# Kernel optimization log

Measured on AMD Instinct MI355X. Metric: run time of the kernel, lower is better.

## Reference

```python
import jax, jax.numpy as jnp
import numpy as np

B, S, V, E, H, T = 256, 160, 50000, 300, 256, 200

def setup_inputs() -> dict:
    key = jax.random.key(0)
    ks = jax.random.split(key, 12)
    return {
        'x1': jax.random.randint(ks[0], (B, S), 0, V),
        'x2': jax.random.randint(ks[1], (B, S), 0, V),
        'x1mask': jnp.ones((B, S), jnp.float32),
        'key_c': jax.random.normal(ks[2], (B, S, T), jnp.float32) * 0.1,
        'key_r': jax.random.normal(ks[3], (B, S, T), jnp.float32) * 0.1,
        'emb_table': jax.random.normal(ks[4], (V, E), jnp.float32) * 0.1,
        'W_ih': jax.random.normal(ks[5], (4 * H, E), jnp.float32) * 0.05,
        'W_hh': jax.random.normal(ks[6], (4 * H, H), jnp.float32) * 0.05,
        'W_kh': jax.random.normal(ks[7], (4 * H, T), jnp.float32) * 0.05,
        'b_g': jnp.zeros((4 * H,), jnp.float32),
        'W_attn': jax.random.normal(ks[8], (H, H), jnp.float32) * 0.05,
        'b_attn': jnp.zeros((H,), jnp.float32),
        'M': jax.random.normal(ks[9], (H, H), jnp.float32) * 0.05,
        'b': jnp.zeros((1,), jnp.float32),
    }

def _run_rnn(x_emb, k_emb, W_ih, W_hh, W_kh, b_g):
    # x_emb: [B,S,E], k_emb: [B,S,T] -> hidden states [B,S,H]
    Bn = x_emb.shape[0]
    h0 = jnp.zeros((Bn, H), x_emb.dtype)
    c0 = jnp.zeros((Bn, H), x_emb.dtype)
    def cell(carry, inp):
        h, c = carry
        x_t, k_t = inp
        g = x_t @ W_ih.T + h @ W_hh.T + k_t @ W_kh.T + b_g  # [B,4H]
        i, f, gg, o = jnp.split(g, 4, axis=-1)
        c = jax.nn.sigmoid(f) * c + jax.nn.sigmoid(i) * jnp.tanh(gg)
        h = jax.nn.sigmoid(o) * jnp.tanh(c)
        return (h, c), h
    xs = (jnp.swapaxes(x_emb, 0, 1), jnp.swapaxes(k_emb, 0, 1))  # time-major
    (_, _), hs = jax.lax.scan(cell, (h0, c0), xs)
    return jnp.swapaxes(hs, 0, 1)  # [B,S,H]

def reference(x1, x2, x1mask, key_c, key_r, emb_table, W_ih, W_hh, W_kh, b_g,
              W_attn, b_attn, M, b):
    x1_emb = emb_table[x1]  # [B,S,E] (dropout = identity at eval)
    x2_emb = emb_table[x2]
    sc = _run_rnn(x1_emb, key_c, W_ih, W_hh, W_kh, b_g)  # context states [B,S,H]
    rs = _run_rnn(x2_emb, key_r, W_ih, W_hh, W_kh, b_g)
    r = rs[:, -1]  # last response hidden [B,H]
    # masked dot-product attention over context states keyed by r
    attn = sc @ W_attn.T + b_attn  # [B,S,H]
    energies = jnp.einsum('bsh,bh->bs', attn, r) * x1mask
    alpha = jax.nn.softmax(energies, axis=-1)
    c_attn = jnp.einsum('bs,bsh->bh', alpha, sc)
    # bilinear score
    o = jnp.einsum('bh,hk,bk->b', c_attn, M, r) + b[0]
    return o
```

## Files before the change

### kernel.cpp

```cpp
#include <hip/hip_runtime.h>
#include <math.h>

#define B_   256
#define S_   160
#define E_   300
#define H_   256
#define T_   200
#define G4H  1024
#define CH   16
#define NCH  10

typedef float  f32x4  __attribute__((ext_vector_type(4)));
typedef __bf16 bf16x4 __attribute__((ext_vector_type(4)));
typedef __bf16 bf16x8 __attribute__((ext_vector_type(8)));

__device__ __forceinline__ float sigf(float x) {
    float e = expf(-fabsf(x));
    float p = 1.0f / (1.0f + e);
    return x >= 0.0f ? p : e * p;
}

__device__ __forceinline__ int norig(int np) {
    return ((np >> 4) & 3) * 256 + ((np >> 6) << 4) + (np & 15);
}

__device__ __forceinline__ float4 pick4(const float* __restrict__ e,
                                        const float* __restrict__ k, int kg) {
    if (kg < E_)      return *(const float4*)(e + kg);
    if (kg < E_ + T_) return *(const float4*)(k + (kg - E_));
    return make_float4(0.f, 0.f, 0.f, 0.f);
}

__device__ __forceinline__ void split4(float4 v, bf16x4& h, bf16x4& l) {
    h[0] = (__bf16)v.x; l[0] = (__bf16)(v.x - (float)h[0]);
    h[1] = (__bf16)v.y; l[1] = (__bf16)(v.y - (float)h[1]);
    h[2] = (__bf16)v.z; l[2] = (__bf16)(v.z - (float)h[2]);
    h[3] = (__bf16)v.w; l[3] = (__bf16)(v.w - (float)h[3]);
}

__global__ __launch_bounds__(128) void prep_split(
    const float* __restrict__ Whh, const float* __restrict__ Wih,
    const float* __restrict__ Wkh,
    __bf16* __restrict__ whh_hi, __bf16* __restrict__ whh_lo,
    __bf16* __restrict__ wik_hi, __bf16* __restrict__ wik_lo)
{
    const int n  = blockIdx.x;
    const int np = ((n & 255) >> 4) * 64 + (n >> 8) * 16 + (n & 15);
    const int t  = threadIdx.x;
    {
        const int k4 = t * 4;
        float4 v;
        if (k4 < E_)            v = *(const float4*)(Wih + (size_t)n * E_ + k4);
        else if (k4 < E_ + T_)  v = *(const float4*)(Wkh + (size_t)n * T_ + (k4 - E_));
        else                    v = make_float4(0.f, 0.f, 0.f, 0.f);
        bf16x4 h, l;
        split4(v, h, l);
        *(bf16x4*)(wik_hi + (size_t)np * 512 + k4) = h;
        *(bf16x4*)(wik_lo + (size_t)np * 512 + k4) = l;
    }
    if (t < 64) {
        const int k4 = t * 4;
        const float4 v = *(const float4*)(Whh + (size_t)n * 256 + k4);
        bf16x4 h, l;
        split4(v, h, l);
        *(bf16x4*)(whh_hi + (size_t)np * 256 + k4) = h;
        *(bf16x4*)(whh_lo + (size_t)np * 256 + k4) = l;
    }
}

__global__ __launch_bounds__(512, 2) void gemm_g2(
    const int* __restrict__ x1, const int* __restrict__ x2,
    const float* __restrict__ key_c, const float* __restrict__ key_r,
    const float* __restrict__ emb,
    const __bf16* __restrict__ wik_hi, const __bf16* __restrict__ wik_lo,
    const float* __restrict__ bg,
    float* __restrict__ G, int s0)
{
    __shared__ __align__(16) __bf16 Ah[128 * 32];
    __shared__ __align__(16) __bf16 Al[128 * 32];
    __shared__ __align__(16) __bf16 Bh[128 * 32];
    __shared__ __align__(16) __bf16 Bl[128 * 32];

    const int t   = threadIdx.x;
    const int rnn = blockIdx.z;
    const int m0  = blockIdx.x * 128;
    const int n0  = blockIdx.y * 128;
    const int* xx = rnn ? x2 : x1;
    const float* key = rnn ? key_r : key_c;

    const int r0 = t >> 2;
    const int cq = t & 3;
    const int csw = ((cq ^ ((r0 >> 1) & 3)) * 16);

    const float* aeb; const float* akb;
    const __bf16* wph; const __bf16* wpl;
    {
        const int am = m0 + r0;
        const int bs = (am >> 4) * S_ + s0 + (am & 15);
        aeb = emb + (size_t)xx[bs] * E_;
        akb = key + (size_t)bs * T_;
        wph = wik_hi + (size_t)(n0 + r0) * 512;
        wpl = wik_lo + (size_t)(n0 + r0) * 512;
    }

    const int w  = t >> 6;
    const int wm = w >> 2;
    const int wn = w & 3;
    const int l  = t & 63;
    const int cl = l & 15;
    const int ch = l >> 4;
    const int chs = ((ch ^ ((cl >> 1) & 3)) * 16);

    f32x4 acc[4][2];
    #pragma unroll
    for (int fm = 0; fm < 4; ++fm)
        #pragma unroll
        for (int fn = 0; fn < 2; ++fn) acc[fm][fn] = (f32x4){0.f, 0.f, 0.f, 0.f};

    for (int kt = 0; kt < 16; ++kt) {
        const int kg = kt * 32 + cq * 8;
        const float4 va0 = pick4(aeb, akb, kg);
        const float4 va1 = pick4(aeb, akb, kg + 4);
        const bf16x8 vbh = *(const bf16x8*)(wph + kg);
        const bf16x8 vbl = *(const bf16x8*)(wpl + kg);
        bf16x4 h0, l0, h1, l1;
        split4(va0, h0, l0);
        split4(va1, h1, l1);
        const bf16x8 sah = __builtin_shufflevector(h0, h1, 0, 1, 2, 3, 4, 5, 6, 7);
        const bf16x8 sal = __builtin_shufflevector(l0, l1, 0, 1, 2, 3, 4, 5, 6, 7);
        __syncthreads();
        {
            const int off = r0 * 64 + csw;
            *(bf16x8*)((char*)Ah + off) = sah;
            *(bf16x8*)((char*)Al + off) = sal;
            *(bf16x8*)((char*)Bh + off) = vbh;
            *(bf16x8*)((char*)Bl + off) = vbl;
        }
        __syncthreads();

        bf16x8 fBh[2], fBl[2];
        #pragma unroll
        for (int fn = 0; fn < 2; ++fn) {
            const int off = (wn * 32 + fn * 16 + cl) * 64 + chs;
            fBh[fn] = *(const bf16x8*)((const char*)Bh + off);
            fBl[fn] = *(const bf16x8*)((const char*)Bl + off);
        }
        #pragma unroll
        for (int fm = 0; fm < 4; ++fm) {
            const int off = (wm * 64 + fm * 16 + cl) * 64 + chs;
            const bf16x8 fAh = *(const bf16x8*)((const char*)Ah + off);
            const bf16x8 fAl = *(const bf16x8*)((const char*)Al + off);
            #pragma unroll
            for (int fn = 0; fn < 2; ++fn) {
                acc[fm][fn] = __builtin_amdgcn_mfma_f32_16x16x32_bf16(fAh, fBh[fn], acc[fm][fn], 0, 0, 0);
                acc[fm][fn] = __builtin_amdgcn_mfma_f32_16x16x32_bf16(fAh, fBl[fn], acc[fm][fn], 0, 0, 0);
                acc[fm][fn] = __builtin_amdgcn_mfma_f32_16x16x32_bf16(fAl, fBh[fn], acc[fm][fn], 0, 0, 0);
            }
        }
    }

    float bgl[2];
    #pragma unroll
    for (int fn = 0; fn < 2; ++fn)
        bgl[fn] = bg[norig(n0 + wn * 32 + fn * 16 + cl)];

    #pragma unroll
    for (int fm = 0; fm < 4; ++fm) {
        #pragma unroll
        for (int r = 0; r < 4; ++r) {
            const int m  = m0 + wm * 64 + fm * 16 + ch * 4 + r;
            const int b  = m >> 4;
            const int sl = m & 15;
            float* rowp = G + ((size_t)(rnn * CH + sl) * B_ + b) * G4H;
            #pragma unroll
            for (int fn = 0; fn < 2; ++fn)
                rowp[n0 + wn * 32 + fn * 16 + cl] = acc[fm][fn][r] + bgl[fn];
        }
    }
}

__global__ __launch_bounds__(512, 2) void lstm_ks(
    const float* __restrict__ G,
    const __bf16* __restrict__ Whi, const __bf16* __restrict__ Wlo,
    const __bf16* __restrict__ hhi_in, const __bf16* __restrict__ hlo_in,
    __bf16* __restrict__ hhi_out, __bf16* __restrict__ hlo_out,
    float* __restrict__ cst, float* __restrict__ sc,
    int sl, int s_glob, int first)
{
    __shared__ float ps[128 * 66];

    const int t  = threadIdx.x;
    const int w  = t >> 6;
    const int l  = t & 63;
    const int cl = l & 15;
    const int ch = l >> 4;
    const int mt = blockIdx.x;
    const int jt = blockIdx.y;
    const int rnn = mt >> 4;
    const int b0  = (mt & 15) * 16;
    const int m0  = mt * 16;

    const int me = (t >> 4) & 15;
    const int jl = t & 15;
    const int j  = jt * 16 + jl;
    float Ge[4];
    float c_in = 0.f;
    if (t < 256) {
        const float* Gb = G + ((size_t)(rnn * CH + sl) * B_ + b0 + me) * G4H + jt * 64;
        #pragma unroll
        for (int g = 0; g < 4; ++g) Ge[g] = Gb[g * 16 + jl];
        if (!first) c_in = cst[(size_t)(m0 + me) * 256 + j];
    }

    const size_t ab = (size_t)(m0 + cl) * 256 + w * 32 + ch * 8;
    const bf16x8 fAh = *(const bf16x8*)(hhi_in + ab);
    const bf16x8 fAl = *(const bf16x8*)(hlo_in + ab);

    bf16x8 fBh[4], fBl[4];
    #pragma unroll
    for (int g = 0; g < 4; ++g) {
        const size_t bb = (size_t)(jt * 64 + g * 16 + cl) * 256 + w * 32 + ch * 8;
        fBh[g] = *(const bf16x8*)(Whi + bb);
        fBl[g] = *(const bf16x8*)(Wlo + bb);
    }

    f32x4 acc[4];
    #pragma unroll
    for (int g = 0; g < 4; ++g) acc[g] = (f32x4){0.f, 0.f, 0.f, 0.f};
    #pragma unroll
    for (int g = 0; g < 4; ++g) {
        acc[g] = __builtin_amdgcn_mfma_f32_16x16x32_bf16(fAh, fBh[g], acc[g], 0, 0, 0);
        acc[g] = __builtin_amdgcn_mfma_f32_16x16x32_bf16(fAh, fBl[g], acc[g], 0, 0, 0);
        acc[g] = __builtin_amdgcn_mfma_f32_16x16x32_bf16(fAl, fBh[g], acc[g], 0, 0, 0);
    }

    #pragma unroll
    for (int g = 0; g < 4; ++g)
        #pragma unroll
        for (int r = 0; r < 4; ++r)
            ps[(w * 16 + ch * 4 + r) * 66 + g * 16 + cl] = acc[g][r];
    __syncthreads();

    if (t < 256) {
        float g4[4];
        #pragma unroll
        for (int g = 0; g < 4; ++g) {
            float s = Ge[g];
            #pragma unroll
            for (int w2 = 0; w2 < 8; ++w2)
                s += ps[(w2 * 16 + me) * 66 + g * 16 + jl];
            g4[g] = s;
        }
        const float c = sigf(g4[1]) * c_in + sigf(g4[0]) * tanhf(g4[2]);
        const float h = sigf(g4[3]) * tanhf(c);
        cst[(size_t)(m0 + me) * 256 + j] = c;
        const __bf16 hh = (__bf16)h;
        const size_t ho = (size_t)(m0 + me) * 256 + j;
        hhi_out[ho] = hh;
        hlo_out[ho] = (__bf16)(h - (float)hh);
        if (rnn == 0)
            sc[((size_t)(b0 + me) * S_ + s_glob) * H_ + j] = h;
    }
}

__global__ __launch_bounds__(256) void final_kernel(
    const float* __restrict__ sc,
    const __bf16* __restrict__ rhi, const __bf16* __restrict__ rlo,
    const float* __restrict__ Wattn, const float* __restrict__ battn,
    const float* __restrict__ M, const float* __restrict__ bscal,
    const float* __restrict__ mask, float* __restrict__ out)
{
    __shared__ float rs[256], us[256], red[256], as_[256];
    const int b = blockIdx.x;
    const int t = threadIdx.x;

    const size_t ri = (size_t)(256 + b) * 256 + t;
    rs[t] = (float)rhi[ri] + (float)rlo[ri];
    __syncthreads();

    float acc = 0.0f;
    for (int h = 0; h < 256; ++h) acc += rs[h] * Wattn[h * 256 + t];
    us[t] = acc;

    red[t] = battn[t] * rs[t];
    __syncthreads();
    for (int off = 128; off; off >>= 1) {
        if (t < off) red[t] += red[t + off];
        __syncthreads();
    }
    float beta = red[0];
    __syncthreads();

    float vh = 0.0f;
    {
        const float* Mrow = M + t * 256;
        for (int k = 0; k < 256; ++k) vh += Mrow[k] * rs[k];
    }

    float e = -INFINITY;
    if (t < S_) {
        float d = 0.0f;
        const float* scrow = sc + ((size_t)b * S_ + t) * H_;
        for (int h = 0; h < 256; ++h) d += scrow[h] * us[h];
        e = (d + beta) * mask[b * S_ + t];
    }
    red[t] = e;
    __syncthreads();
    for (int off = 128; off; off >>= 1) {
        if (t < off) red[t] = fmaxf(red[t], red[t + off]);
        __syncthreads();
    }
    float mx = red[0];
    __syncthreads();

    float p = (t < S_) ? expf(e - mx) : 0.0f;
    as_[t] = p;
    red[t] = p;
    __syncthreads();
    for (int off = 128; off; off >>= 1) {
        if (t < off) red[t] += red[t + off];
        __syncthreads();
    }
    float inv = 1.0f / red[0];
    __syncthreads();

    float ca = 0.0f;
    for (int s = 0; s < S_; ++s) ca += as_[s] * sc[((size_t)b * S_ + s) * H_ + t];
    ca *= inv;

    red[t] = ca * vh;
    __syncthreads();
    for (int off = 128; off; off >>= 1) {
        if (t < off) red[t] += red[t + off];
        __syncthreads();
    }
    if (t == 0) out[b] = red[0] + bscal[0];
}

extern "C" void kernel_launch(void* const* d_in, const int* in_sizes, int n_in,
                              void* d_out, int out_size, void* d_ws, size_t ws_size,
                              hipStream_t stream)
{
    const int*   x1    = (const int*)d_in[0];
    const int*   x2    = (const int*)d_in[1];
    const float* mask  = (const float*)d_in[2];
    const float* key_c = (const float*)d_in[3];
    const float* key_r = (const float*)d_in[4];
    const float* emb   = (const float*)d_in[5];
    const float* Wih   = (const float*)d_in[6];
    const float* Whh   = (const float*)d_in[7];
    const float* Wkh   = (const float*)d_in[8];
    const float* bg    = (const float*)d_in[9];
    const float* Wattn = (const float*)d_in[10];
    const float* battn = (const float*)d_in[11];
    const float* M     = (const float*)d_in[12];
    const float* bb    = (const float*)d_in[13];
    float* out = (float*)d_out;
    char*  wsb = (char*)d_ws;

    float*  G     = (float*)(wsb + 0);
    float*  sc    = (float*)(wsb + 33554432);
    __bf16* hhi0  = (__bf16*)(wsb + 75497472);
    __bf16* hlo0  = (__bf16*)(wsb + 75759616);
    __bf16* hhi1  = (__bf16*)(wsb + 76021760);
    __bf16* hlo1  = (__bf16*)(wsb + 76283904);
    float*  cst   = (float*)(wsb + 76546048);
    __bf16* WhhHi = (__bf16*)(wsb + 77070336);
    __bf16* WhhLo = (__bf16*)(wsb + 77594624);
    __bf16* WikHi = (__bf16*)(wsb + 78118912);
    __bf16* WikLo = (__bf16*)(wsb + 79167488);
    if (ws_size < 80216064) return;

    hipMemsetAsync(hhi0, 0, 524288, stream);
    prep_split<<<dim3(1024), 128, 0, stream>>>(Whh, Wih, Wkh,
                                               WhhHi, WhhLo, WikHi, WikLo);

    for (int ci = 0; ci < NCH; ++ci) {
        gemm_g2<<<dim3(32, 8, 2), 512, 0, stream>>>(x1, x2, key_c, key_r, emb,
                                                    WikHi, WikLo, bg, G, ci * CH);
        for (int slq = 0; slq < CH; ++slq) {
            const int s   = ci * CH + slq;
            const int par = s & 1;
            lstm_ks<<<dim3(32, 16), 512, 0, stream>>>(G, WhhHi, WhhLo,
                                                      par ? hhi1 : hhi0,
                                                      par ? hlo1 : hlo0,
                                                      par ? hhi0 : hhi1,
                                                      par ? hlo0 : hlo1,
                                                      cst, sc, slq, s, s == 0);
        }
    }

    final_kernel<<<dim3(256), 256, 0, stream>>>(sc, hhi0, hlo0, Wattn, battn,
                                                M, bb, mask, out);
}
```

Baseline: 1.508 ms.

## Use single-wave LSTM step blocks and widen GEMM K-tile to 64

The recurrent step kernel is rewritten so one 64-thread wave computes a full 16x64 gate tile over the whole K=256 reduction, instead of 8 waves each doing a K-slice and reducing partials through shared memory with a barrier. This drops the LDS reduction and block sync from the latency-bound per-timestep kernel, at the cost of a longer serial MFMA chain per wave and fewer threads per block. Separately, the input-projection GEMM now stages 64-wide K tiles with a new XOR swizzle, halving the number of barrier-separated iterations in exchange for more LDS.

New measurement: 1.901 ms. 26.1% more time.

```diff
diff --git a/kernel.cpp b/kernel.cpp
--- a/kernel.cpp
+++ b/kernel.cpp
@@ -76,10 +76,10 @@
     const float* __restrict__ bg,
     float* __restrict__ G, int s0)
 {
-    __shared__ __align__(16) __bf16 Ah[128 * 32];
-    __shared__ __align__(16) __bf16 Al[128 * 32];
-    __shared__ __align__(16) __bf16 Bh[128 * 32];
-    __shared__ __align__(16) __bf16 Bl[128 * 32];
+    __shared__ __align__(16) __bf16 Ah[128 * 64];
+    __shared__ __align__(16) __bf16 Al[128 * 64];
+    __shared__ __align__(16) __bf16 Bh[128 * 64];
+    __shared__ __align__(16) __bf16 Bl[128 * 64];
 
     const int t   = threadIdx.x;
     const int rnn = blockIdx.z;
@@ -90,7 +90,8 @@
 
     const int r0 = t >> 2;
     const int cq = t & 3;
-    const int csw = ((cq ^ ((r0 >> 1) & 3)) * 16);
+    const int p0 = (cq ^ (r0 & 7)) * 16;
+    const int p1 = ((cq + 4) ^ (r0 & 7)) * 16;
 
     const float* aeb; const float* akb;
     const __bf16* wph; const __bf16* wpl;
@@ -109,7 +110,6 @@
     const int l  = t & 63;
     const int cl = l & 15;
     const int ch = l >> 4;
-    const int chs = ((ch ^ ((cl >> 1) & 3)) * 16);
 
     f32x4 acc[4][2];
     #pragma unroll
@@ -117,44 +117,64 @@
         #pragma unroll
         for (int fn = 0; fn < 2; ++fn) acc[fm][fn] = (f32x4){0.f, 0.f, 0.f, 0.f};
 
-    for (int kt = 0; kt < 16; ++kt) {
-        const int kg = kt * 32 + cq * 8;
-        const float4 va0 = pick4(aeb, akb, kg);
-        const float4 va1 = pick4(aeb, akb, kg + 4);
-        const bf16x8 vbh = *(const bf16x8*)(wph + kg);
-        const bf16x8 vbl = *(const bf16x8*)(wpl + kg);
-        bf16x4 h0, l0, h1, l1;
-        split4(va0, h0, l0);
-        split4(va1, h1, l1);
-        const bf16x8 sah = __builtin_shufflevector(h0, h1, 0, 1, 2, 3, 4, 5, 6, 7);
-        const bf16x8 sal = __builtin_shufflevector(l0, l1, 0, 1, 2, 3, 4, 5, 6, 7);
+    for (int kt = 0; kt < 8; ++kt) {
+        const int kg0 = kt * 64 + cq * 8;
+        const int kg1 = kg0 + 32;
+        const float4 va0 = pick4(aeb, akb, kg0);
+        const float4 va1 = pick4(aeb, akb, kg0 + 4);
+        const float4 va2 = pick4(aeb, akb, kg1);
+        const float4 va3 = pick4(aeb, akb, kg1 + 4);
+        const bf16x8 vbh0 = *(const bf16x8*)(wph + kg0);
+        const bf16x8 vbh1 = *(const bf16x8*)(wph + kg1);
+        const bf16x8 vbl0 = *(const bf16x8*)(wpl + kg0);
+        const bf16x8 vbl1 = *(const bf16x8*)(wpl + kg1);
+        bf16x4 h0, l0, h1, l1, h2, l2, h3, l3;
+        split4(va0, h0, l0); split4(va1, h1, l1);
+        split4(va2, h2, l2); split4(va3, h3, l3);
+        const bf16x8 sah0 = __builtin_shufflevector(h0, h1, 0, 1, 2, 3, 4, 5, 6, 7);
+        const bf16x8 sal0 = __builtin_shufflevector(l0, l1, 0, 1, 2, 3, 4, 5, 6, 7);
+        const bf16x8 sah1 = __builtin_shufflevector(h2, h3, 0, 1, 2, 3, 4, 5, 6, 7);
+        const bf16x8 sal1 = __builtin_shufflevector(l2, l3, 0, 1, 2, 3, 4, 5, 6, 7);
         __syncthreads();
         {
-            const int off = r0 * 64 + csw;
-            *(bf16x8*)((char*)Ah + off) = sah;
-            *(bf16x8*)((char*)Al + off) = sal;
-            *(bf16x8*)((char*)Bh + off) = vbh;
-            *(bf16x8*)((char*)Bl + off) = vbl;
+            char* a = (char*)Ah + r0 * 128;
+            char* b = (char*)Bh + r0 * 128;
+            char* a2 = (char*)Al + r0 * 128;
+            char* b2 = (char*)Bl + r0 * 128;
+            *(bf16x8*)(a + p0)  = sah0;
+            *(bf16x8*)(a + p1)  = sah1;
+            *(bf16x8*)(a2 + p0) = sal0;
+            *(bf16x8*)(a2 + p1) = sal1;
+            *(bf16x8*)(b + p0)  = vbh0;
+            *(bf16x8*)(b + p1)  = vbh1;
+            *(bf16x8*)(b2 + p0) = vbl0;
+            *(bf16x8*)(b2 + p1) = vbl1;
         }
         __syncthreads();
 
-        bf16x8 fBh[2], fBl[2];
-        #pragma unroll
-        for (int fn = 0; fn < 2; ++fn) {
-            const int off = (wn * 32 + fn * 16 + cl) * 64 + chs;
-            fBh[fn] = *(const bf16x8*)((const char*)Bh + off);
-            fBl[fn] = *(const bf16x8*)((const char*)Bl + off);
-        }
-        #pragma unroll
-        for (int fm = 0; fm < 4; ++fm) {
-            const int off = (wm * 64 + fm * 16 + cl) * 64 + chs;
-            const bf16x8 fAh = *(const bf16x8*)((const char*)Ah + off);
-            const bf16x8 fAl = *(const bf16x8*)((const char*)Al + off);
+        #pragma unroll
+        for (int s = 0; s < 2; ++s) {
+            const int c = s * 4 + ch;
+            bf16x8 fBh[2], fBl[2];
             #pragma unroll
             for (int fn = 0; fn < 2; ++fn) {
-                acc[fm][fn] = __builtin_amdgcn_mfma_f32_16x16x32_bf16(fAh, fBh[fn], acc[fm][fn], 0, 0, 0);
-                acc[fm][fn] = __builtin_amdgcn_mfma_f32_16x16x32_bf16(fAh, fBl[fn], acc[fm][fn], 0, 0, 0);
-                acc[fm][fn] = __builtin_amdgcn_mfma_f32_16x16x32_bf16(fAl, fBh[fn], acc[fm][fn], 0, 0, 0);
+                const int row = wn * 32 + fn * 16 + cl;
+                const int off = row * 128 + (c ^ (row & 7)) * 16;
+                fBh[fn] = *(const bf16x8*)((const char*)Bh + off);
+                fBl[fn] = *(const bf16x8*)((const char*)Bl + off);
+            }
+            #pragma unroll
+            for (int fm = 0; fm < 4; ++fm) {
+                const int row = wm * 64 + fm * 16 + cl;
+                const int off = row * 128 + (c ^ (row & 7)) * 16;
+                const bf16x8 fAh = *(const bf16x8*)((const char*)Ah + off);
+                const bf16x8 fAl = *(const bf16x8*)((const char*)Al + off);
+                #pragma unroll
+                for (int fn = 0; fn < 2; ++fn) {
+                    acc[fm][fn] = __builtin_amdgcn_mfma_f32_16x16x32_bf16(fAh, fBh[fn], acc[fm][fn], 0, 0, 0);
+                    acc[fm][fn] = __builtin_amdgcn_mfma_f32_16x16x32_bf16(fAh, fBl[fn], acc[fm][fn], 0, 0, 0);
+                    acc[fm][fn] = __builtin_amdgcn_mfma_f32_16x16x32_bf16(fAl, fBh[fn], acc[fm][fn], 0, 0, 0);
+                }
             }
         }
     }
@@ -179,7 +199,7 @@
     }
 }
 
-__global__ __launch_bounds__(512, 2) void lstm_ks(
+__global__ __launch_bounds__(64) void lstm_dir(
     const float* __restrict__ G,
     const __bf16* __restrict__ Whi, const __bf16* __restrict__ Wlo,
     const __bf16* __restrict__ hhi_in, const __bf16* __restrict__ hlo_in,
@@ -187,79 +207,76 @@
     float* __restrict__ cst, float* __restrict__ sc,
     int sl, int s_glob, int first)
 {
-    __shared__ float ps[128 * 66];
-
-    const int t  = threadIdx.x;
-    const int w  = t >> 6;
-    const int l  = t & 63;
+    const int l  = threadIdx.x;
     const int cl = l & 15;
     const int ch = l >> 4;
-    const int mt = blockIdx.x;
-    const int jt = blockIdx.y;
+    const int bid = blockIdx.x;
+    const int mt  = bid >> 4;
+    const int jt  = bid & 15;
     const int rnn = mt >> 4;
     const int b0  = (mt & 15) * 16;
     const int m0  = mt * 16;
-
-    const int me = (t >> 4) & 15;
-    const int jl = t & 15;
-    const int j  = jt * 16 + jl;
-    float Ge[4];
-    float c_in = 0.f;
-    if (t < 256) {
-        const float* Gb = G + ((size_t)(rnn * CH + sl) * B_ + b0 + me) * G4H + jt * 64;
-        #pragma unroll
-        for (int g = 0; g < 4; ++g) Ge[g] = Gb[g * 16 + jl];
-        if (!first) c_in = cst[(size_t)(m0 + me) * 256 + j];
-    }
-
-    const size_t ab = (size_t)(m0 + cl) * 256 + w * 32 + ch * 8;
-    const bf16x8 fAh = *(const bf16x8*)(hhi_in + ab);
-    const bf16x8 fAl = *(const bf16x8*)(hlo_in + ab);
-
-    bf16x8 fBh[4], fBl[4];
-    #pragma unroll
-    for (int g = 0; g < 4; ++g) {
-        const size_t bb = (size_t)(jt * 64 + g * 16 + cl) * 256 + w * 32 + ch * 8;
-        fBh[g] = *(const bf16x8*)(Whi + bb);
-        fBl[g] = *(const bf16x8*)(Wlo + bb);
-    }
+    const int j   = jt * 16 + cl;
+
+    bf16x8 fAh[8], fAl[8];
+    const size_t ab = (size_t)(m0 + cl) * 256 + ch * 8;
+    #pragma unroll
+    for (int ks = 0; ks < 8; ++ks) {
+        fAh[ks] = *(const bf16x8*)(hhi_in + ab + ks * 32);
+        fAl[ks] = *(const bf16x8*)(hlo_in + ab + ks * 32);
+    }
+
+    float Ge[4][4];
+    const float* Gb = G + ((size_t)(rnn * CH + sl) * B_ + b0 + ch * 4) * G4H + jt * 64;
+    #pragma unroll
+    for (int r = 0; r < 4; ++r)
+        #pragma unroll
+        for (int g = 0; g < 4; ++g)
+            Ge[g][r] = Gb[(size_t)r * G4H + g * 16 + cl];
+    float c_in[4];
+    #pragma unroll
+    for (int r = 0; r < 4; ++r)
+        c_in[r] = first ? 0.f : cst[(size_t)(m0 + ch * 4 + r) * 256 + j];
 
     f32x4 acc[4];
     #pragma unroll
     for (int g = 0; g < 4; ++g) acc[g] = (f32x4){0.f, 0.f, 0.f, 0.f};
-    #pragma unroll
-    for (int g = 0; g < 4; ++g) {
-        acc[g] = __builtin_amdgcn_mfma_f32_16x16x32_bf16(fAh, fBh[g], acc[g], 0, 0, 0);
-        acc[g] = __builtin_amdgcn_mfma_f32_16x16x32_bf16(fAh, fBl[g], acc[g], 0, 0, 0);
-        acc[g] = __builtin_amdgcn_mfma_f32_16x16x32_bf16(fAl, fBh[g], acc[g], 0, 0, 0);
-    }
-
-    #pragma unroll
-    for (int g = 0; g < 4; ++g)
-        #pragma unroll
-        for (int r = 0; r < 4; ++r)
-            ps[(w * 16 + ch * 4 + r) * 66 + g * 16 + cl] = acc[g][r];
-    __syncthreads();
-
-    if (t < 256) {
-        float g4[4];
+
+    #pragma unroll
+    for (int ks = 0; ks < 8; ++ks) {
+        bf16x8 fBh[4], fBl[4];
         #pragma unroll
         for (int g = 0; g < 4; ++g) {
-            float s = Ge[g];
-            #pragma unroll
-            for (int w2 = 0; w2 < 8; ++w2)
-                s += ps[(w2 * 16 + me) * 66 + g * 16 + jl];
-            g4[g] = s;
+            const size_t bb = (size_t)(jt * 64 + g * 16 + cl) * 256 + ks * 32 + ch * 8;
+            fBh[g] = *(const bf16x8*)(Whi + bb);
+            fBl[g] = *(const bf16x8*)(Wlo + bb);
         }
-        const float c = sigf(g4[1]) * c_in + sigf(g4[0]) * tanhf(g4[2]);
-        const float h = sigf(g4[3]) * tanhf(c);
-        cst[(size_t)(m0 + me) * 256 + j] = c;
+        #pragma unroll
+        for (int g = 0; g < 4; ++g)
+            acc[g] = __builtin_amdgcn_mfma_f32_16x16x32_bf16(fAh[ks], fBh[g], acc[g], 0, 0, 0);
+        #pragma unroll
+        for (int g = 0; g < 4; ++g)
+            acc[g] = __builtin_amdgcn_mfma_f32_16x16x32_bf16(fAh[ks], fBl[g], acc[g], 0, 0, 0);
+        #pragma unroll
+        for (int g = 0; g < 4; ++g)
+            acc[g] = __builtin_amdgcn_mfma_f32_16x16x32_bf16(fAl[ks], fBh[g], acc[g], 0, 0, 0);
+    }
+
+    #pragma unroll
+    for (int r = 0; r < 4; ++r) {
+        const float gi = acc[0][r] + Ge[0][r];
+        const float gf = acc[1][r] + Ge[1][r];
+        const float gg = acc[2][r] + Ge[2][r];
+        const float go = acc[3][r] + Ge[3][r];
+        const float c = sigf(gf) * c_in[r] + sigf(gi) * tanhf(gg);
+        const float h = sigf(go) * tanhf(c);
+        cst[(size_t)(m0 + ch * 4 + r) * 256 + j] = c;
         const __bf16 hh = (__bf16)h;
-        const size_t ho = (size_t)(m0 + me) * 256 + j;
+        const size_t ho = (size_t)(m0 + ch * 4 + r) * 256 + j;
         hhi_out[ho] = hh;
         hlo_out[ho] = (__bf16)(h - (float)hh);
         if (rnn == 0)
-            sc[((size_t)(b0 + me) * S_ + s_glob) * H_ + j] = h;
+            sc[((size_t)(b0 + ch * 4 + r) * S_ + s_glob) * H_ + j] = h;
     }
 }
 
@@ -381,12 +398,12 @@
         for (int slq = 0; slq < CH; ++slq) {
             const int s   = ci * CH + slq;
             const int par = s & 1;
-            lstm_ks<<<dim3(32, 16), 512, 0, stream>>>(G, WhhHi, WhhLo,
-                                                      par ? hhi1 : hhi0,
-                                                      par ? hlo1 : hlo0,
-                                                      par ? hhi0 : hhi1,
-                                                      par ? hlo0 : hlo1,
-                                                      cst, sc, slq, s, s == 0);
+            lstm_dir<<<dim3(512), 64, 0, stream>>>(G, WhhHi, WhhLo,
+                                                   par ? hhi1 : hhi0,
+                                                   par ? hlo1 : hlo0,
+                                                   par ? hhi0 : hhi1,
+                                                   par ? hlo0 : hlo1,
+                                                   cst, sc, slq, s, s == 0);
         }
     }
 
```
